# Optimization experiments

Measured on AMD Instinct MI355X. Metric: run time of the kernel, lower is better.

Reference implementation:

```python
import jax, jax.numpy as jnp
import numpy as np

N = 100000
E = 800000
IN_CH = 128
HID = 32
HEADS = 8
OUT_CH = 40
NEG_SLOPE = 0.2


def setup_inputs() -> dict:
    key = jax.random.key(0)
    ks = jax.random.split(key, 10)
    x = jax.random.normal(ks[0], (N, IN_CH), dtype=jnp.float32)
    edge_index = jax.random.randint(ks[1], (2, E), 0, N, dtype=jnp.int64)
    # GATConv layer 1: in -> heads*hid, concat=True
    s1 = 1.0 / np.sqrt(IN_CH)
    W1 = jax.random.uniform(ks[2], (IN_CH, HEADS * HID), jnp.float32, -s1, s1)
    att_src1 = jax.random.uniform(ks[3], (1, HEADS, HID), jnp.float32, -s1, s1)
    att_dst1 = jax.random.uniform(ks[4], (1, HEADS, HID), jnp.float32, -s1, s1)
    b1 = jnp.zeros((HEADS * HID,), jnp.float32)
    # GATConv layer 2: heads*hid -> out, heads=1, concat=True
    s2 = 1.0 / np.sqrt(HEADS * HID)
    W2 = jax.random.uniform(ks[5], (HEADS * HID, OUT_CH), jnp.float32, -s2, s2)
    att_src2 = jax.random.uniform(ks[6], (1, 1, OUT_CH), jnp.float32, -s2, s2)
    att_dst2 = jax.random.uniform(ks[7], (1, 1, OUT_CH), jnp.float32, -s2, s2)
    b2 = jnp.zeros((OUT_CH,), jnp.float32)
    return {"x": x, "edge_index": edge_index,
            "W1": W1, "att_src1": att_src1, "att_dst1": att_dst1, "b1": b1,
            "W2": W2, "att_src2": att_src2, "att_dst2": att_dst2, "b2": b2}


def _gat_layer(x, src, dst, W, att_src, att_dst, bias, heads, out_ch):
    n = x.shape[0]
    xp = (x @ W).reshape(n, heads, out_ch)               # [N,H,C]
    a_src = jnp.sum(xp * att_src, axis=-1)               # [N,H]
    a_dst = jnp.sum(xp * att_dst, axis=-1)               # [N,H]
    logits = a_src[src] + a_dst[dst]                      # [Etot,H]
    logits = jnp.where(logits > 0, logits, NEG_SLOPE * logits)  # leaky_relu
    # segment softmax over destination node
    m = jax.ops.segment_max(logits, dst, num_segments=n)  # [N,H]
    p = jnp.exp(logits - m[dst])
    z = jax.ops.segment_sum(p, dst, num_segments=n)
    alpha = p / (z[dst] + 1e-16)                           # [Etot,H]
    out = jax.ops.segment_sum(xp[src] * alpha[:, :, None], dst, num_segments=n)
    return out.reshape(n, heads * out_ch) + bias


def reference(x, edge_index, W1, att_src1, att_dst1, b1, W2, att_src2, att_dst2, b2):
    n = x.shape[0]
    # add self loops (PyG GATConv default add_self_loops=True)
    loop = jnp.arange(n, dtype=edge_index.dtype)
    src = jnp.concatenate([edge_index[0], loop])
    dst = jnp.concatenate([edge_index[1], loop])
    # dropout p=0.2 is identity in eval mode
    h = _gat_layer(x, src, dst, W1, att_src1, att_dst1, b1, HEADS, HID)
    h = jax.nn.relu(h)
    out = _gat_layer(h, src, dst, W2, att_src2, att_dst2, b2, 1, OUT_CH)
    return jax.nn.log_softmax(out, axis=1)
```

## Files before the change

kernel.cpp:

```cpp
#include <hip/hip_runtime.h>
#include <math.h>

#define NN 100000
#define NE 800000
#define C1 256
#define OC 40
#define XPAD 64
#define NEG 0.2f
#define FCHUNK 4096

typedef _Float16 h4 __attribute__((ext_vector_type(4)));
typedef _Float16 h8 __attribute__((ext_vector_type(8)));
typedef float f4v __attribute__((ext_vector_type(4)));
typedef float f2v __attribute__((ext_vector_type(2)));

static __device__ __forceinline__ float leaky(float v){ return v > 0.f ? v : NEG*v; }

static __device__ __forceinline__ h8 mk8(float4 a, float4 b){
  h8 r = {(_Float16)a.x,(_Float16)a.y,(_Float16)a.z,(_Float16)a.w,
          (_Float16)b.x,(_Float16)b.y,(_Float16)b.z,(_Float16)b.w};
  return r;
}

static __device__ __forceinline__ void gload_lds16(const float* g, float* l){
  __builtin_amdgcn_global_load_lds((const __attribute__((address_space(1))) void*)g,
                                   (__attribute__((address_space(3))) void*)l, 16, 0, 0);
}


__global__ __launch_bounds__(256) void k_wt(const float* __restrict__ W1, const float* __restrict__ W2,
                                            const float* __restrict__ aS1, const float* __restrict__ aD1,
                                            const float* __restrict__ aS2, const float* __restrict__ aD2,
                                            _Float16* __restrict__ W1t, _Float16* __restrict__ W2t){
  int b = blockIdx.x;
  if (b < 128){
    int k = b, nb = threadIdx.x;
    W1t[(size_t)nb*128 + k] = (_Float16)W1[k*256 + nb];
  } else if (b < 176){
    int nb = b - 128;
    int e = threadIdx.x;
    int l = e >> 2, j = e & 3;
    int k = (l>>5)*128 + ((l>>4)&1)*64 + j*16 + (l&15);
    float v = (nb < OC) ? W2[(size_t)k*OC + nb] : 0.f;
    W2t[(size_t)nb*256 + e] = (_Float16)v;
  } else if (b < 178){
    int b2 = b - 176;
    int h  = threadIdx.x >> 5;
    int kb = (threadIdx.x & 31) * 4;
    const float* att = b2 ? aD1 : aS1;
    #pragma unroll
    for (int kk = 0; kk < 4; ++kk){
      int k = kb + kk;
      float s = 0.f;
      for (int c = 0; c < 32; ++c) s += W1[k*256 + h*32 + c] * att[h*32 + c];
      W1t[(size_t)(256 + b2*8 + h)*128 + k] = (_Float16)s;
    }
  } else {
    int j = b - 178;
    int e = threadIdx.x;
    int l = e >> 2, jj = e & 3;
    int k = (l>>5)*128 + ((l>>4)&1)*64 + jj*16 + (l&15);
    float v = 0.f;
    if (j == 0){ for (int c = 0; c < OC; ++c) v += W2[(size_t)k*OC + c] * aS2[c]; }
    else if (j == 1){ for (int c = 0; c < OC; ++c) v += W2[(size_t)k*OC + c] * aD2[c]; }
    W2t[(size_t)(48 + j)*256 + e] = (_Float16)v;
  }
}

__global__ __launch_bounds__(256) void k_gemm1(const float* __restrict__ x,
    const _Float16* __restrict__ W1t, unsigned* __restrict__ xp1w,
    float* __restrict__ asrc, float* __restrict__ adst)
{
  __shared__ float xs[64*128];
  const int tid  = threadIdx.x;
  const int lane = tid & 63;
  const int w    = tid >> 6;
  const int wr = w >> 1, wc = w & 1;
  const int n = lane & 15, quad = lane >> 4;
  const int r0 = blockIdx.x * 64;

  if (r0 + 64 <= NN){
    #pragma unroll
    for (int it = 0; it < 8; ++it){
      int idx = it*256 + tid;
      int row = idx >> 5, c16 = idx & 31;
      const float* src = x + (size_t)(r0 + row)*128 + ((c16 ^ (row & 7)) << 2);
      gload_lds16(src, xs + ((size_t)(it*256 + w*64) << 2));
    }
  } else {
    #pragma unroll
    for (int it = 0; it < 8; ++it){
      int idx = it*256 + tid;
      int row = idx >> 5, c16 = idx & 31;
      int gr = r0 + row; gr = gr < NN ? gr : NN-1;
      ((float4*)xs)[idx] = *(const float4*)(x + (size_t)gr*128 + ((c16 ^ (row & 7)) << 2));
    }
  }

  h8 b0[9];
  #pragma unroll
  for (int ct = 0; ct < 8; ++ct)
    b0[ct] = *(const h8*)(W1t + (size_t)(wc*128 + ct*16 + n)*128 + quad*8);
  if (wc == 0) b0[8] = *(const h8*)(W1t + (size_t)(256 + n)*128 + quad*8);

  __syncthreads();

  f4v acc[2][8];
  #pragma unroll
  for (int rt = 0; rt < 2; ++rt)
    #pragma unroll
    for (int ct = 0; ct < 8; ++ct) acc[rt][ct] = (f4v){0.f,0.f,0.f,0.f};
  f4v accE0 = {0.f,0.f,0.f,0.f}, accE1 = {0.f,0.f,0.f,0.f};

  const int rowA = wr*32 + n;
  const int rowB = rowA + 16;
  const int s = n & 7;

  #pragma unroll
  for (int ks = 0; ks < 4; ++ks){
    const int base16 = ks*8 + quad*2;
    float4 fa0 = ((const float4*)xs)[rowA*32 + ((base16    ) ^ s)];
    float4 fa1 = ((const float4*)xs)[rowA*32 + ((base16 + 1) ^ s)];
    float4 fb0 = ((const float4*)xs)[rowB*32 + ((base16    ) ^ s)];
    float4 fb1 = ((const float4*)xs)[rowB*32 + ((base16 + 1) ^ s)];
    h8 a0 = mk8(fa0, fa1);
    h8 a1 = mk8(fb0, fb1);
    #pragma unroll
    for (int ct = 0; ct < 8; ++ct){
      h8 b = (ks == 0) ? b0[ct]
           : *(const h8*)(W1t + (size_t)(wc*128 + ct*16 + n)*128 + ks*32 + quad*8);
      acc[0][ct] = __builtin_amdgcn_mfma_f32_16x16x32_f16(a0, b, acc[0][ct], 0, 0, 0);
      acc[1][ct] = __builtin_amdgcn_mfma_f32_16x16x32_f16(a1, b, acc[1][ct], 0, 0, 0);
    }
    if (wc == 0){
      h8 b = (ks == 0) ? b0[8]
           : *(const h8*)(W1t + (size_t)(256 + n)*128 + ks*32 + quad*8);
      accE0 = __builtin_amdgcn_mfma_f32_16x16x32_f16(a0, b, accE0, 0, 0, 0);
      accE1 = __builtin_amdgcn_mfma_f32_16x16x32_f16(a1, b, accE1, 0, 0, 0);
    }
  }

  #pragma unroll
  for (int rt = 0; rt < 2; ++rt){
    #pragma unroll
    for (int reg = 0; reg < 4; ++reg){
      const int row = r0 + wr*32 + rt*16 + quad*4 + reg;
      if (row < NN){
        float v[8];
        #pragma unroll
        for (int ct = 0; ct < 8; ++ct) v[ct] = acc[rt][ct][reg];
        unsigned dwA = (unsigned)__builtin_amdgcn_cvt_pk_fp8_f32(v[0], v[1], 0, false);
        dwA = (unsigned)__builtin_amdgcn_cvt_pk_fp8_f32(v[2], v[3], (int)dwA, true);
        unsigned dwB = (unsigned)__builtin_amdgcn_cvt_pk_fp8_f32(v[4], v[5], 0, false);
        dwB = (unsigned)__builtin_amdgcn_cvt_pk_fp8_f32(v[6], v[7], (int)dwB, true);
        unsigned* xr = xp1w + (size_t)row*64 + wc*32 + n;
        xr[0]  = dwA;
        xr[16] = dwB;
        if (wc == 0){
          float vE = (rt == 0) ? accE0[reg] : accE1[reg];
          if (n < 8) asrc[row*8 + n] = vE;
          else       adst[row*8 + (n - 8)] = vE;
        }
      }
    }
  }
}

__global__ __launch_bounds__(256) void k_deg_init(int* deg){
  int i = blockIdx.x*256 + threadIdx.x;
  if (i < NN) deg[i] = 1;
}
__global__ __launch_bounds__(256) void k_deg_count(const int* __restrict__ ei, int* deg){
  int i = blockIdx.x*256 + threadIdx.x;
  if (i < NE) atomicAdd(&deg[ei[NE + i]], 1);
}
__global__ __launch_bounds__(256) void k_scan1(const int* __restrict__ deg, int* part, int* bsum){
  __shared__ int lds[256];
  const int t = threadIdx.x;
  const int base = blockIdx.x*1024;
  int v[4]; int s = 0;
  #pragma unroll
  for (int i = 0; i < 4; ++i){ int idx = base + t*4 + i; v[i] = (idx < NN) ? deg[idx] : 0; s += v[i]; }
  lds[t] = s; __syncthreads();
  for (int off = 1; off < 256; off <<= 1){
    int xx = (t >= off) ? lds[t-off] : 0;
    __syncthreads();
    lds[t] += xx;
    __syncthreads();
  }
  int excl = lds[t] - s;
  #pragma unroll
  for (int i = 0; i < 4; ++i){ int idx = base + t*4 + i; if (idx < NN) part[idx] = excl; excl += v[i]; }
  if (t == 255) bsum[blockIdx.x] = lds[255];
}
__global__ void k_scan2(const int* __restrict__ bsum, int* boff){
  const int l = threadIdx.x;
  int a = (l      < 98) ? bsum[l]      : 0;
  int b = (64 + l < 98) ? bsum[64 + l] : 0;
  int sa = a, sb = b;
  #pragma unroll
  for (int off = 1; off < 64; off <<= 1){
    int ta = __shfl_up(sa, off, 64);
    int tb = __shfl_up(sb, off, 64);
    if (l >= off){ sa += ta; sb += tb; }
  }
  const int totalA = __shfl(sa, 63, 64);
  if (l      < 98) boff[l]      = sa - a;
  if (64 + l < 98) boff[64 + l] = totalA + sb - b;
}
__global__ __launch_bounds__(256) void k_scan3(const int* __restrict__ part, const int* __restrict__ boff,
                                               int* rowptr, int* cursor){
  int i = blockIdx.x*256 + threadIdx.x;
  if (i < NN){ int v = part[i] + boff[i >> 10]; rowptr[i] = v; cursor[i] = v; }
  if (i == 0) rowptr[NN] = NN + NE;
}
__global__ __launch_bounds__(256) void k_fill(const int* __restrict__ ei, int* cursor, int* __restrict__ esrc){
  const int xcd = blockIdx.x & 7;
  const int base = (blockIdx.x >> 3) * FCHUNK;
  const int lo = xcd * (NN/8), hi = lo + (NN/8);
  const int end = (base + FCHUNK < NE + NN) ? (base + FCHUNK) : (NE + NN);
  for (int i = base + threadIdx.x; i < end; i += 256){
    int s, d;
    if (i < NE){ s = ei[i]; d = ei[NE + i]; } else { s = d = i - NE; }
    if (d >= lo && d < hi){
      int slot = atomicAdd(&cursor[d], 1);
      esrc[slot] = s;
    }
  }
}

template<int B>
static __device__ __forceinline__ void agg1_batch(
    const int j0, const int je, const int lane,
    const int* __restrict__ esrc, const float* __restrict__ asrc,
    const float adA, const float adB,
    const unsigned* __restrict__ xp1w,
    f2v& accLo, f2v& accHi, float& z0, float& z1)
{
  const int cnt = je - j0;
  const int slot = lane & 15;
  const int hA = (lane >> 4) << 1;
  int idx = j0 + slot; idx = idx < je ? idx : je - 1;
  const int sv = esrc[idx];
  float pv0 = 0.f, pv1 = 0.f;
  if (slot < cnt){
    f2v av = *(const f2v*)(asrc + (size_t)sv*8 + hA);
    pv0 = __expf(leaky(av.x + adA));
    pv1 = __expf(leaky(av.y + adB));
  }
  z0 += pv0; z1 += pv1;
  unsigned u[B];
  #pragma unroll
  for (int e = 0; e < B; ++e){
    int s = __builtin_amdgcn_readlane(sv, e);
    u[e] = xp1w[(size_t)s*64 + lane];
  }
  __builtin_amdgcn_sched_barrier(0);
  const int pb = lane & 48;
  #pragma unroll
  for (int e = 0; e < B; ++e){
    const float pA = __shfl(pv0, pb | e, 64);
    const float pB = __shfl(pv1, pb | e, 64);
    f2v lo = __builtin_amdgcn_cvt_pk_f32_fp8((int)u[e], false);
    f2v hi = __builtin_amdgcn_cvt_pk_f32_fp8((int)u[e], true);
    accLo += (f2v){pA, pA} * lo;
    accHi += (f2v){pB, pB} * hi;
  }
}

__global__ __launch_bounds__(256) void k_agg1(const unsigned* __restrict__ xp1w,
    const float* __restrict__ asrc, const float* __restrict__ adst,
    const float* __restrict__ b1, const int* __restrict__ rowptr,
    const int* __restrict__ esrc, _Float16* __restrict__ h1)
{
  const int lane = threadIdx.x & 63;
  int n = __builtin_amdgcn_readfirstlane(blockIdx.x*4 + (threadIdx.x >> 6));
  const int hA = (lane >> 4) << 1;
  const f2v ad = *(const f2v*)(adst + (size_t)n*8 + hA);
  const int jb = rowptr[n], je = rowptr[n+1];
  const int cbase = (lane>>5)*128 + ((lane>>4)&1)*64 + (lane&15);
  const float bp0 = b1[cbase], bp1 = b1[cbase+16], bp2 = b1[cbase+32], bp3 = b1[cbase+48];
  f2v accLo = {0.f,0.f}, accHi = {0.f,0.f};
  float z0 = 0.f, z1 = 0.f;

  int j0 = jb;
  while (j0 < je){
    if (je - j0 > 8){
      agg1_batch<16>(j0, je, lane, esrc, asrc, ad.x, ad.y, xp1w, accLo, accHi, z0, z1);
      j0 += 16;
    } else {
      agg1_batch<8>(j0, je, lane, esrc, asrc, ad.x, ad.y, xp1w, accLo, accHi, z0, z1);
      j0 += 8;
    }
  }
  #pragma unroll
  for (int off = 1; off <= 8; off <<= 1){
    z0 += __shfl_xor(z0, off, 64);
    z1 += __shfl_xor(z1, off, 64);
  }
  const float invA = 1.f/(z0 + 1e-16f), invB = 1.f/(z1 + 1e-16f);
  h4 o = {(_Float16)fmaxf(accLo.x*invA + bp0, 0.f),
          (_Float16)fmaxf(accLo.y*invA + bp1, 0.f),
          (_Float16)fmaxf(accHi.x*invB + bp2, 0.f),
          (_Float16)fmaxf(accHi.y*invB + bp3, 0.f)};
  ((h4*)h1)[(size_t)n*64 + lane] = o;
}

__global__ __launch_bounds__(256) void k_gemm2(const _Float16* __restrict__ h1,
    const _Float16* __restrict__ W2t, _Float16* __restrict__ xp2,
    float* __restrict__ asrc2, float* __restrict__ adst2)
{
  const int tid  = threadIdx.x;
  const int lane = tid & 63;
  const int w    = tid >> 6;
  const int n = lane & 15, quad = lane >> 4;
  const int r0 = blockIdx.x * 64 + w*16;

  f4v acc[4];
  #pragma unroll
  for (int ct = 0; ct < 4; ++ct) acc[ct] = (f4v){0.f,0.f,0.f,0.f};

  int rr = r0 + n; rr = rr < NN ? rr : NN-1;

  #pragma unroll
  for (int ks = 0; ks < 8; ++ks){
    h8 a = *(const h8*)(h1 + (size_t)rr*256 + ks*32 + quad*8);
    #pragma unroll
    for (int ct = 0; ct < 4; ++ct){
      h8 b = *(const h8*)(W2t + (size_t)(ct*16 + n)*256 + ks*32 + quad*8);
      acc[ct] = __builtin_amdgcn_mfma_f32_16x16x32_f16(a, b, acc[ct], 0, 0, 0);
    }
  }

  #pragma unroll
  for (int reg = 0; reg < 4; ++reg){
    const int row = r0 + quad*4 + reg;
    if (row < NN){
      float v0 = acc[0][reg], v1 = acc[1][reg], v2 = acc[2][reg], v3 = acc[3][reg];
      _Float16* xr = xp2 + (size_t)row*XPAD + n;
      xr[0]  = (_Float16)v0;
      xr[16] = (_Float16)v1;
      if (n < 8) xr[32] = (_Float16)v2;
      if (n == 0) asrc2[row] = v3;
      if (n == 1) adst2[row] = v3;
    }
  }
}

__global__ __launch_bounds__(256) void k_agg2(const _Float16* __restrict__ xp2,
    const float* __restrict__ asrc2, const float* __restrict__ adst2,
    const float* __restrict__ b2, const int* __restrict__ rowptr,
    const int* __restrict__ esrc, float* __restrict__ out)
{
  const int lane = threadIdx.x & 63;
  int n = __builtin_amdgcn_readfirstlane(blockIdx.x*4 + (threadIdx.x >> 6));
  const float ad = adst2[n];
  const int jb = rowptr[n], je = rowptr[n+1];
  const bool act = lane < OC;
  float acc = 0.f, zacc = 0.f;

  for (int j0 = jb; j0 < je; j0 += 16) {
    const int cnt = je - j0;
    int idx = j0 + (lane & 15); idx = idx < je ? idx : je - 1;
    const int sv = esrc[idx];
    const float pv = (lane < cnt && lane < 16)
                   ? __expf(leaky(asrc2[sv] + ad)) : 0.f;
    zacc += pv;
    _Float16 u[16];
    #pragma unroll
    for (int e = 0; e < 16; ++e){
      int s = __builtin_amdgcn_readlane(sv, e);
      u[e] = xp2[(size_t)s*XPAD + lane];
    }
    __builtin_amdgcn_sched_barrier(0);
    #pragma unroll
    for (int e = 0; e < 16; ++e){
      const float p = __shfl(pv, e, 64);
      acc += p * (float)u[e];
    }
  }
  #pragma unroll
  for (int off = 1; off < 64; off <<= 1) zacc += __shfl_xor(zacc, off, 64);

  float val = act ? (acc/(zacc + 1e-16f) + b2[lane]) : -INFINITY;
  float m = val;
  #pragma unroll
  for (int off = 32; off > 0; off >>= 1) m = fmaxf(m, __shfl_xor(m, off, 64));
  float e = act ? __expf(val - m) : 0.f;
  float sum = e;
  #pragma unroll
  for (int off = 32; off > 0; off >>= 1) sum += __shfl_xor(sum, off, 64);
  if (act) out[(size_t)n*OC + lane] = val - m - __logf(sum);
}

extern "C" void kernel_launch(void* const* d_in, const int* in_sizes, int n_in,
                              void* d_out, int out_size, void* d_ws, size_t ws_size,
                              hipStream_t stream)
{
  const float* x   = (const float*)d_in[0];
  const int*   ei  = (const int*)  d_in[1];
  const float* W1  = (const float*)d_in[2];
  const float* aS1 = (const float*)d_in[3];
  const float* aD1 = (const float*)d_in[4];
  const float* b1  = (const float*)d_in[5];
  const float* W2  = (const float*)d_in[6];
  const float* aS2 = (const float*)d_in[7];
  const float* aD2 = (const float*)d_in[8];
  const float* b2  = (const float*)d_in[9];
  float* out = (float*)d_out;

  char* wsp = (char*)d_ws;
  size_t off = 0;
  auto alloc = [&](size_t bytes){ void* p = wsp + off; off += (bytes + 255) & ~(size_t)255; return p; };
  unsigned* xp1w = (unsigned*)alloc((size_t)NN*C1);
  _Float16* h1  = (_Float16*)alloc((size_t)NN*C1*2);
  float* as1  = (float*)alloc((size_t)NN*8*4);
  float* ad1  = (float*)alloc((size_t)NN*8*4);
  float* as2  = (float*)alloc((size_t)NN*4);
  float* ad2  = (float*)alloc((size_t)NN*4);
  int* deg    = (int*)alloc((size_t)NN*4);
  int* part   = (int*)alloc((size_t)NN*4);
  int* rowptr = (int*)alloc((size_t)(NN+1)*4);
  int* cursor = (int*)alloc((size_t)NN*4);
  int* bsum   = (int*)alloc(98*4);
  int* boff   = (int*)alloc(98*4);
  int* esrc   = (int*)alloc((size_t)(NN+NE)*4);
  _Float16* W1t = (_Float16*)alloc((size_t)272*128*2);
  _Float16* W2t = (_Float16*)alloc((size_t)64*256*2);
  _Float16* xp2 = (_Float16*)alloc((size_t)NN*XPAD*2);
  (void)ws_size; (void)in_sizes; (void)n_in; (void)out_size;

  const int fill_chunks = (NE + NN + FCHUNK - 1) / FCHUNK;

  k_wt       <<<194,  256, 0, stream>>>(W1, W2, aS1, aD1, aS2, aD2, W1t, W2t);
  k_gemm1    <<<1563, 256, 0, stream>>>(x, W1t, xp1w, as1, ad1);
  k_deg_init <<<391,  256, 0, stream>>>(deg);
  k_deg_count<<<3125, 256, 0, stream>>>(ei, deg);
  k_scan1    <<<98,   256, 0, stream>>>(deg, part, bsum);
  k_scan2    <<<1,    64,  0, stream>>>(bsum, boff);
  k_scan3    <<<391,  256, 0, stream>>>(part, boff, rowptr, cursor);
  k_fill     <<<fill_chunks*8, 256, 0, stream>>>(ei, cursor, esrc);
  k_agg1     <<<25000,256, 0, stream>>>(xp1w, as1, ad1, b1, rowptr, esrc, h1);
  k_gemm2    <<<1563, 256, 0, stream>>>(h1, W2t, xp2, as2, ad2);
  k_agg2     <<<25000,256, 0, stream>>>(xp2, as2, ad2, b2, rowptr, esrc, out);
}
```

Before: 348.1 us.

## Fold degree init/count into weight-prep and GEMM1 launches; vectorize agg2 gathers

```diff
diff --git a/kernel.cpp b/kernel.cpp
--- a/kernel.cpp
+++ b/kernel.cpp
@@ -8,6 +8,7 @@
 #define XPAD 64
 #define NEG 0.2f
 #define FCHUNK 4096
+#define G1BLK 1563
 
 typedef _Float16 h4 __attribute__((ext_vector_type(4)));
 typedef _Float16 h8 __attribute__((ext_vector_type(8)));
@@ -31,7 +32,8 @@
 __global__ __launch_bounds__(256) void k_wt(const float* __restrict__ W1, const float* __restrict__ W2,
                                             const float* __restrict__ aS1, const float* __restrict__ aD1,
                                             const float* __restrict__ aS2, const float* __restrict__ aD2,
-                                            _Float16* __restrict__ W1t, _Float16* __restrict__ W2t){
+                                            _Float16* __restrict__ W1t, _Float16* __restrict__ W2t,
+                                            int* __restrict__ deg){
   int b = blockIdx.x;
   if (b < 128){
     int k = b, nb = threadIdx.x;
@@ -55,7 +57,7 @@
       for (int c = 0; c < 32; ++c) s += W1[k*256 + h*32 + c] * att[h*32 + c];
       W1t[(size_t)(256 + b2*8 + h)*128 + k] = (_Float16)s;
     }
-  } else {
+  } else if (b < 194){
     int j = b - 178;
     int e = threadIdx.x;
     int l = e >> 2, jj = e & 3;
@@ -64,14 +66,23 @@
     if (j == 0){ for (int c = 0; c < OC; ++c) v += W2[(size_t)k*OC + c] * aS2[c]; }
     else if (j == 1){ for (int c = 0; c < OC; ++c) v += W2[(size_t)k*OC + c] * aD2[c]; }
     W2t[(size_t)(48 + j)*256 + e] = (_Float16)v;
+  } else {
+    int i = (b - 194)*256 + threadIdx.x;
+    if (i < NN) deg[i] = 1;
   }
 }
 
 __global__ __launch_bounds__(256) void k_gemm1(const float* __restrict__ x,
     const _Float16* __restrict__ W1t, unsigned* __restrict__ xp1w,
-    float* __restrict__ asrc, float* __restrict__ adst)
+    float* __restrict__ asrc, float* __restrict__ adst,
+    const int* __restrict__ ei, int* __restrict__ deg)
 {
   __shared__ float xs[64*128];
+  if (blockIdx.x >= G1BLK){
+    int i = (blockIdx.x - G1BLK)*256 + threadIdx.x;
+    if (i < NE) atomicAdd(&deg[ei[NE + i]], 1);
+    return;
+  }
   const int tid  = threadIdx.x;
   const int lane = tid & 63;
   const int w    = tid >> 6;
@@ -166,14 +177,6 @@
   }
 }
 
-__global__ __launch_bounds__(256) void k_deg_init(int* deg){
-  int i = blockIdx.x*256 + threadIdx.x;
-  if (i < NN) deg[i] = 1;
-}
-__global__ __launch_bounds__(256) void k_deg_count(const int* __restrict__ ei, int* deg){
-  int i = blockIdx.x*256 + threadIdx.x;
-  if (i < NE) atomicAdd(&deg[ei[NE + i]], 1);
-}
 __global__ __launch_bounds__(256) void k_scan1(const int* __restrict__ deg, int* part, int* bsum){
   __shared__ int lds[256];
   const int t = threadIdx.x;
@@ -353,44 +356,61 @@
     const int* __restrict__ esrc, float* __restrict__ out)
 {
   const int lane = threadIdx.x & 63;
+  const int g = lane >> 4;
+  const int t = lane & 15;
   int n = __builtin_amdgcn_readfirstlane(blockIdx.x*4 + (threadIdx.x >> 6));
   const float ad = adst2[n];
   const int jb = rowptr[n], je = rowptr[n+1];
-  const bool act = lane < OC;
-  float acc = 0.f, zacc = 0.f;
-
-  for (int j0 = jb; j0 < je; j0 += 16) {
+  f4v acc = {0.f,0.f,0.f,0.f};
+  float zacc = 0.f;
+
+  for (int j0 = jb; j0 < je; j0 += 16){
     const int cnt = je - j0;
-    int idx = j0 + (lane & 15); idx = idx < je ? idx : je - 1;
+    int idx = j0 + t; idx = idx < je ? idx : je - 1;
     const int sv = esrc[idx];
-    const float pv = (lane < cnt && lane < 16)
-                   ? __expf(leaky(asrc2[sv] + ad)) : 0.f;
+    const float pv = (t < cnt) ? __expf(leaky(asrc2[sv] + ad)) : 0.f;
     zacc += pv;
-    _Float16 u[16];
-    #pragma unroll
-    for (int e = 0; e < 16; ++e){
-      int s = __builtin_amdgcn_readlane(sv, e);
-      u[e] = xp2[(size_t)s*XPAD + lane];
+    h4 u[4];
+    #pragma unroll
+    for (int e4 = 0; e4 < 4; ++e4){
+      int svg = __shfl(sv, e4*4 + g, 64);
+      u[e4] = *(const h4*)(xp2 + (size_t)svg*XPAD + t*4);
     }
     __builtin_amdgcn_sched_barrier(0);
     #pragma unroll
-    for (int e = 0; e < 16; ++e){
-      const float p = __shfl(pv, e, 64);
-      acc += p * (float)u[e];
-    }
-  }
-  #pragma unroll
-  for (int off = 1; off < 64; off <<= 1) zacc += __shfl_xor(zacc, off, 64);
-
-  float val = act ? (acc/(zacc + 1e-16f) + b2[lane]) : -INFINITY;
-  float m = val;
-  #pragma unroll
-  for (int off = 32; off > 0; off >>= 1) m = fmaxf(m, __shfl_xor(m, off, 64));
-  float e = act ? __expf(val - m) : 0.f;
-  float sum = e;
-  #pragma unroll
-  for (int off = 32; off > 0; off >>= 1) sum += __shfl_xor(sum, off, 64);
-  if (act) out[(size_t)n*OC + lane] = val - m - __logf(sum);
+    for (int e4 = 0; e4 < 4; ++e4){
+      const float p = __shfl(pv, e4*4 + g, 64);
+      acc.x += p*(float)u[e4].x;
+      acc.y += p*(float)u[e4].y;
+      acc.z += p*(float)u[e4].z;
+      acc.w += p*(float)u[e4].w;
+    }
+  }
+  #pragma unroll
+  for (int off = 1; off <= 8; off <<= 1) zacc += __shfl_xor(zacc, off, 64);
+  #pragma unroll
+  for (int off = 16; off <= 32; off <<= 1){
+    acc.x += __shfl_xor(acc.x, off, 64);
+    acc.y += __shfl_xor(acc.y, off, 64);
+    acc.z += __shfl_xor(acc.z, off, 64);
+    acc.w += __shfl_xor(acc.w, off, 64);
+  }
+  const float inv = 1.f/(zacc + 1e-16f);
+  const bool act = t < 10;
+  float4 bv = act ? *(const float4*)(b2 + 4*t) : make_float4(0.f,0.f,0.f,0.f);
+  float v0 = acc.x*inv + bv.x, v1 = acc.y*inv + bv.y;
+  float v2 = acc.z*inv + bv.z, v3 = acc.w*inv + bv.w;
+  float m = act ? fmaxf(fmaxf(v0,v1), fmaxf(v2,v3)) : -INFINITY;
+  #pragma unroll
+  for (int off = 1; off <= 8; off <<= 1) m = fmaxf(m, __shfl_xor(m, off, 64));
+  float es = act ? (__expf(v0-m)+__expf(v1-m)+__expf(v2-m)+__expf(v3-m)) : 0.f;
+  #pragma unroll
+  for (int off = 1; off <= 8; off <<= 1) es += __shfl_xor(es, off, 64);
+  if (lane < 10){
+    float lse = m + __logf(es);
+    float4 o = make_float4(v0-lse, v1-lse, v2-lse, v3-lse);
+    *(float4*)(out + (size_t)n*OC + 4*t) = o;
+  }
 }
 
 extern "C" void kernel_launch(void* const* d_in, const int* in_sizes, int n_in,
@@ -431,16 +451,15 @@
   (void)ws_size; (void)in_sizes; (void)n_in; (void)out_size;
 
   const int fill_chunks = (NE + NN + FCHUNK - 1) / FCHUNK;
-
-  k_wt       <<<194,  256, 0, stream>>>(W1, W2, aS1, aD1, aS2, aD2, W1t, W2t);
-  k_gemm1    <<<1563, 256, 0, stream>>>(x, W1t, xp1w, as1, ad1);
-  k_deg_init <<<391,  256, 0, stream>>>(deg);
-  k_deg_count<<<3125, 256, 0, stream>>>(ei, deg);
-  k_scan1    <<<98,   256, 0, stream>>>(deg, part, bsum);
-  k_scan2    <<<1,    64,  0, stream>>>(bsum, boff);
-  k_scan3    <<<391,  256, 0, stream>>>(part, boff, rowptr, cursor);
-  k_fill     <<<fill_chunks*8, 256, 0, stream>>>(ei, cursor, esrc);
-  k_agg1     <<<25000,256, 0, stream>>>(xp1w, as1, ad1, b1, rowptr, esrc, h1);
-  k_gemm2    <<<1563, 256, 0, stream>>>(h1, W2t, xp2, as2, ad2);
-  k_agg2     <<<25000,256, 0, stream>>>(xp2, as2, ad2, b2, rowptr, esrc, out);
-}
+  const int deg_blocks  = (NE + 255) / 256;
+
+  k_wt    <<<194 + (NN + 255)/256, 256, 0, stream>>>(W1, W2, aS1, aD1, aS2, aD2, W1t, W2t, deg);
+  k_gemm1 <<<G1BLK + deg_blocks,   256, 0, stream>>>(x, W1t, xp1w, as1, ad1, ei, deg);
+  k_scan1 <<<98,   256, 0, stream>>>(deg, part, bsum);
+  k_scan2 <<<1,    64,  0, stream>>>(bsum, boff);
+  k_scan3 <<<391,  256, 0, stream>>>(part, boff, rowptr, cursor);
+  k_fill  <<<fill_chunks*8, 256, 0, stream>>>(ei, cursor, esrc);
+  k_agg1  <<<25000,256, 0, stream>>>(xp1w, as1, ad1, b1, rowptr, esrc, h1);
+  k_gemm2 <<<1563, 256, 0, stream>>>(h1, W2t, xp2, as2, ad2);
+  k_agg2  <<<25000,256, 0, stream>>>(xp2, as2, ad2, b2, rowptr, esrc, out);
+}
```

Result: faster. 337.5 us (-3.1%).
